# Optimization experiments

Hardware: AMD Instinct MI355X
Metric: run time of the kernel (lower is better)

Reference implementation:

```python
import jax, jax.numpy as jnp
import numpy as np

EMBED = 256
HEADS = 8
LEVELS = 4
POINTS = 4
HD = EMBED // HEADS  # 32
SHAPES = np.array([[100, 100], [50, 50], [25, 25], [13, 13]], dtype=np.int64)  # (H_l, W_l)


def setup_inputs() -> dict:
    key = jax.random.key(0)
    ks = jax.random.split(key, 12)
    nv = int(SHAPES.prod(-1).sum())  # 13294
    bs, nq, d = 2, nv, EMBED
    level_start = np.concatenate([[0], SHAPES.prod(-1).cumsum()[:-1]])
    s = 0.02
    return {
        "query": jax.random.normal(ks[0], (bs, nq, d), jnp.float32),
        "reference_points": jax.random.uniform(ks[1], (bs, nq, LEVELS, 2), jnp.float32),
        "value": jax.random.normal(ks[2], (bs, nv, d), jnp.float32),
        "spatial_shapes": jnp.asarray(SHAPES, jnp.int32),
        "level_start_index": jnp.asarray(level_start, jnp.int32),
        "key_padding_mask": jnp.zeros((bs, nv), jnp.bool_),
        "W_samp": jax.random.normal(ks[3], (HEADS * LEVELS * POINTS * 2, d), jnp.float32) * s,
        "b_samp": jax.random.normal(ks[4], (HEADS * LEVELS * POINTS * 2,), jnp.float32),
        "W_attn": jax.random.normal(ks[5], (HEADS * LEVELS * POINTS, d), jnp.float32) * s,
        "b_attn": jnp.zeros((HEADS * LEVELS * POINTS,), jnp.float32),
        "W_val": jax.random.normal(ks[6], (d, d), jnp.float32) * s,
        "b_val": jnp.zeros((d,), jnp.float32),
        "W_out": jax.random.normal(ks[7], (d, d), jnp.float32) * s,
        "b_out": jnp.zeros((d,), jnp.float32),
    }


def _msda_core(value_bhnd, shapes_np, starts_np, loc, attn):
    """value_bhnd: (bs, H, nv, hd); loc: (bs, nq, H, L, P, 2) in [0,1]; attn: (bs, nq, H, L, P)."""
    bs, heads, nv, hd = value_bhnd.shape
    nq = loc.shape[1]
    out = jnp.zeros((bs, nq, heads, hd), value_bhnd.dtype)
    for l in range(LEVELS):
        H, W = int(shapes_np[l, 0]), int(shapes_np[l, 1])
        start = int(starts_np[l])
        v = jax.lax.dynamic_slice_in_dim(value_bhnd, start, H * W, axis=2)  # (bs, heads, H*W, hd)
        # grid_sample(align_corners=False): pixel coord = loc * size - 0.5
        lx = loc[:, :, :, l, :, 0] * W - 0.5  # (bs, nq, heads, P)
        ly = loc[:, :, :, l, :, 1] * H - 0.5
        x0 = jnp.floor(lx)
        y0 = jnp.floor(ly)
        tx = lx - x0
        ty = ly - y0
        x0i = x0.astype(jnp.int32)
        y0i = y0.astype(jnp.int32)
        samp = jnp.zeros((bs, heads, nq, POINTS, hd), value_bhnd.dtype)
        for dy, wy in ((0, 1.0 - ty), (1, ty)):
            for dx, wx in ((0, 1.0 - tx), (1, tx)):
                xi = x0i + dx
                yi = y0i + dy
                valid = (xi >= 0) & (xi < W) & (yi >= 0) & (yi < H)  # zeros padding
                idx = jnp.clip(yi, 0, H - 1) * W + jnp.clip(xi, 0, W - 1)  # (bs, nq, heads, P)
                idx_t = idx.transpose(0, 2, 1, 3).reshape(bs, heads, nq * POINTS)
                g = jnp.take_along_axis(v, idx_t[..., None], axis=2)
                g = g.reshape(bs, heads, nq, POINTS, hd)
                w = jnp.where(valid, wx * wy, 0.0).transpose(0, 2, 1, 3)[..., None]
                samp = samp + g * w
        out = out + jnp.einsum("bhqpd,bqhp->bqhd", samp, attn[:, :, :, l, :])
    return out.reshape(bs, nq, heads * hd)


def reference(query, reference_points, value, spatial_shapes, level_start_index,
              key_padding_mask, W_samp, b_samp, W_attn, b_attn, W_val, b_val, W_out, b_out):
    bs, nq, d = query.shape
    v = value @ W_val.T + b_val
    v = jnp.where(key_padding_mask[..., None], 0.0, v)
    v = v.reshape(bs, -1, HEADS, HD).transpose(0, 2, 1, 3)  # (bs, heads, nv, hd)
    off = (query @ W_samp.T + b_samp).reshape(bs, nq, HEADS, LEVELS, POINTS, 2)
    attn = (query @ W_attn.T + b_attn).reshape(bs, nq, HEADS, LEVELS * POINTS)
    attn = jax.nn.softmax(attn, axis=-1).reshape(bs, nq, HEADS, LEVELS, POINTS)
    ss = np.asarray(spatial_shapes)
    starts = np.asarray(level_start_index)
    # offset normalizer is (W, H) per level
    norm = jnp.asarray(ss[:, ::-1].copy(), jnp.float32)
    loc = reference_points[:, :, None, :, None, :] + off / norm[None, None, None, :, None, :]
    out = _msda_core(v, ss, starts, loc, attn)
    return out @ W_out.T + b_out
```

## Files before the change

kernel.cpp:

```cpp
#include <hip/hip_runtime.h>
#include <hip/hip_bf16.h>
#include <hip/hip_fp16.h>
#include <cstdint>
#include <cstddef>

#define EMBED  256
#define NV_PER_B 13294
#define M_PAD   26624
#define NQPB   8

__constant__ const int c_H[4]  = {100, 50, 25, 13};
__constant__ const int c_W[4]  = {100, 50, 25, 13};
__constant__ const int c_ST[4] = {0, 10000, 12500, 13125};

typedef __attribute__((ext_vector_type(8))) short bf16x8;
typedef __attribute__((ext_vector_type(4))) float f32x4;

__device__ inline short f2bf(float x) {
    __hip_bfloat16 h = __float2bfloat16(x);
    return *reinterpret_cast<short*>(&h);
}

__global__ __launch_bounds__(256) void convert_kernel(
    const float* __restrict__ q,  const float* __restrict__ v,
    const float* __restrict__ wv, const float* __restrict__ wsamp,
    const float* __restrict__ wattn, const float* __restrict__ wo,
    const float* __restrict__ bsamp, const float* __restrict__ battn,
    short* __restrict__ q_bf, short* __restrict__ v_bf,
    short* __restrict__ wv_bf, short* __restrict__ wcat_bf,
    short* __restrict__ wo_bf, float* __restrict__ bias_cat,
    int n_real4, int n_pad4)
{
    const int i = blockIdx.x * 256 + threadIdx.x;
    if (i < n_pad4) {
        float4 a = make_float4(0.f, 0.f, 0.f, 0.f);
        float4 b = make_float4(0.f, 0.f, 0.f, 0.f);
        if (i < n_real4) {
            a = ((const float4*)q)[i];
            b = ((const float4*)v)[i];
        }
        ((short4*)q_bf)[i] = make_short4(f2bf(a.x), f2bf(a.y), f2bf(a.z), f2bf(a.w));
        ((short4*)v_bf)[i] = make_short4(f2bf(b.x), f2bf(b.y), f2bf(b.z), f2bf(b.w));
    }
    if (i < 16384) {
        float4 a = ((const float4*)wv)[i];
        float4 c = ((const float4*)wo)[i];
        ((short4*)wv_bf)[i] = make_short4(f2bf(a.x), f2bf(a.y), f2bf(a.z), f2bf(a.w));
        ((short4*)wo_bf)[i] = make_short4(f2bf(c.x), f2bf(c.y), f2bf(c.z), f2bf(c.w));
    }
    if (i < 24576) {
        float4 a = (i < 16384) ? ((const float4*)wsamp)[i]
                               : ((const float4*)wattn)[i - 16384];
        ((short4*)wcat_bf)[i] = make_short4(f2bf(a.x), f2bf(a.y), f2bf(a.z), f2bf(a.w));
    }
    if (i < 96) {
        float4 a = (i < 64) ? ((const float4*)bsamp)[i]
                            : ((const float4*)battn)[i - 64];
        ((float4*)bias_cat)[i] = a;
    }
}

__device__ __forceinline__ void gemm_kloop(
    const short* __restrict__ A, const short* __restrict__ Wt,
    int bm, int bn, char* smem, f32x4 (&acc)[4][4],
    int t, int wave, int lane)
{
    constexpr int K = 256;
    const int row0 = t >> 2, row1 = row0 + 64;
    const int kbl  = t & 3;
    const int kbg0 = kbl ^ (row0 & 3);
    const int kbg1 = kbl ^ (row1 & 3);
    const size_t a0 = (size_t)(bm + row0) * K + kbg0 * 8;
    const size_t a1 = (size_t)(bm + row1) * K + kbg1 * 8;
    const size_t b0 = (size_t)(bn + row0) * K + kbg0 * 8;
    const size_t b1 = (size_t)(bn + row1) * K + kbg1 * 8;
    const int lr16 = lane & 15, qk = lane >> 4;
    const int swz  = (qk ^ (lr16 & 3)) * 16;
    const int wrow = wave & 1, wcol = wave >> 1;

    auto issue = [&](int stage, int k0) {
        char* sa = smem + stage * 16384 + wave * 1024;
        char* sb = sa + 8192;
        __builtin_amdgcn_global_load_lds(
            (const __attribute__((address_space(1))) void*)(A + a0 + k0),
            (__attribute__((address_space(3))) void*)(sa), 16, 0, 0);
        __builtin_amdgcn_global_load_lds(
            (const __attribute__((address_space(1))) void*)(A + a1 + k0),
            (__attribute__((address_space(3))) void*)(sa + 4096), 16, 0, 0);
        __builtin_amdgcn_global_load_lds(
            (const __attribute__((address_space(1))) void*)(Wt + b0 + k0),
            (__attribute__((address_space(3))) void*)(sb), 16, 0, 0);
        __builtin_amdgcn_global_load_lds(
            (const __attribute__((address_space(1))) void*)(Wt + b1 + k0),
            (__attribute__((address_space(3))) void*)(sb + 4096), 16, 0, 0);
    };

    issue(0, 0);
    #pragma unroll
    for (int it = 0; it < 8; ++it) {
        __syncthreads();
        if (it + 1 < 8) issue((it + 1) & 1, (it + 1) * 32);
        const char* sa = smem + (it & 1) * 16384;
        const char* sb = sa + 8192;
        bf16x8 af[4], bfr[4];
        #pragma unroll
        for (int mi = 0; mi < 4; ++mi)
            af[mi] = *(const bf16x8*)(sa + (wrow * 64 + mi * 16 + lr16) * 64 + swz);
        #pragma unroll
        for (int ni = 0; ni < 4; ++ni)
            bfr[ni] = *(const bf16x8*)(sb + (wcol * 64 + ni * 16 + lr16) * 64 + swz);
        #pragma unroll
        for (int mi = 0; mi < 4; ++mi)
            #pragma unroll
            for (int ni = 0; ni < 4; ++ni)
                acc[mi][ni] = __builtin_amdgcn_mfma_f32_16x16x32_bf16(
                    af[mi], bfr[ni], acc[mi][ni], 0, 0, 0);
    }
}

__global__ __launch_bounds__(256) void gemm_mega_kernel(
    const short* __restrict__ v_bf, const short* __restrict__ wv_bf,
    const float* __restrict__ b_val, __half* __restrict__ vproj,
    const short* __restrict__ q_bf, const short* __restrict__ wcat_bf,
    const float* __restrict__ bias_cat, __half* __restrict__ qo)
{
    __shared__ __align__(16) char smem[36864];
    const int t = threadIdx.x;
    const int wave = t >> 6, lane = t & 63;
    const int lr16 = lane & 15, qk = lane >> 4;
    const int wrow = wave & 1, wcol = wave >> 1;
    const int y = blockIdx.y;
    const int bm = blockIdx.x * 128;

    const short* A; const short* Wt; const float* bias; __half* Cc; int Nst, bn;
    if (y < 2) { A = v_bf; Wt = wv_bf;   bias = b_val;    Cc = vproj; Nst = 256; bn = y * 128; }
    else       { A = q_bf; Wt = wcat_bf; bias = bias_cat; Cc = qo;    Nst = 384; bn = (y - 2) * 128; }

    f32x4 acc[4][4] = {};
    gemm_kloop(A, Wt, bm, bn, smem, acc, t, wave, lane);

    __syncthreads();
    __half* ep = (__half*)(smem + wave * 9216);
    const int colbase = bn + wcol * 64;
    float bv[4];
    #pragma unroll
    for (int ni = 0; ni < 4; ++ni) bv[ni] = bias[colbase + ni * 16 + lr16];
    #pragma unroll
    for (int mi = 0; mi < 4; ++mi)
        #pragma unroll
        for (int ni = 0; ni < 4; ++ni)
            #pragma unroll
            for (int r = 0; r < 4; ++r)
                ep[(mi * 16 + qk * 4 + r) * 72 + ni * 16 + lr16] =
                    __float2half(acc[mi][ni][r] + bv[ni]);
    __syncthreads();
    const int er = lane >> 3, ec = (lane & 7) * 8;
    #pragma unroll
    for (int pass = 0; pass < 8; ++pass) {
        const int r = pass * 8 + er;
        const int4 vv = *(const int4*)&ep[r * 72 + ec];
        const int grow = bm + wrow * 64 + r;
        *(int4*)&Cc[(size_t)grow * Nst + colbase + ec] = vv;
    }
}

__global__ __launch_bounds__(256) void gemm_out_kernel(
    const short* __restrict__ corebf, const short* __restrict__ wo_bf,
    const float* __restrict__ b_out, float* __restrict__ C, int M)
{
    __shared__ __align__(16) char smem[36864];
    const int t = threadIdx.x;
    const int wave = t >> 6, lane = t & 63;
    const int lr16 = lane & 15, qk = lane >> 4;
    const int wrow = wave & 1, wcol = wave >> 1;
    const int bm = blockIdx.x * 128, bn = blockIdx.y * 128;

    f32x4 acc[4][4] = {};
    gemm_kloop(corebf, wo_bf, bm, bn, smem, acc, t, wave, lane);

    const int colbase = bn + wcol * 64;
    float bv[4];
    #pragma unroll
    for (int ni = 0; ni < 4; ++ni) bv[ni] = b_out[colbase + ni * 16 + lr16];
    float* ep = (float*)(smem + wave * 8704);
    #pragma unroll
    for (int p = 0; p < 2; ++p) {
        __syncthreads();
        #pragma unroll
        for (int mh = 0; mh < 2; ++mh) {
            const int mi = p * 2 + mh;
            #pragma unroll
            for (int ni = 0; ni < 4; ++ni)
                #pragma unroll
                for (int r = 0; r < 4; ++r)
                    ep[(mh * 16 + qk * 4 + r) * 68 + ni * 16 + lr16] =
                        acc[mi][ni][r] + bv[ni];
        }
        __syncthreads();
        const int er = lane >> 4, ec = (lane & 15) * 4;
        #pragma unroll
        for (int j = 0; j < 8; ++j) {
            const int r = j * 4 + er;
            const float4 vv = *(const float4*)&ep[r * 68 + ec];
            const int grow = bm + wrow * 64 + p * 32 + r;
            if (grow < M)
                *(float4*)&C[(size_t)grow * 256 + colbase + ec] = vv;
        }
    }
}

__global__ __launch_bounds__(256) void msda_core_kernel(
    const __half* __restrict__ vproj,
    const float* __restrict__ refp,
    const __half* __restrict__ qo,
    short* __restrict__ core,
    int nq, int nv, int M)
{
    const int bq0 = blockIdx.x * NQPB;
    const int t = threadIdx.x;

    __shared__ float s_w[NQPB * 128];
    __shared__ float s_ref[NQPB * 8];
    __shared__ unsigned int s_tap[NQPB * 8][65];

    #pragma unroll
    for (int i = 0; i < 4; ++i) {
        const int s = t + i * 256;
        const int q = s >> 7, r = s & 127;
        s_w[s] = __half2float(qo[(size_t)(bq0 + q) * 384 + 256 + r]);
    }
    if (t < NQPB * 8) {
        const int gq = min(bq0 + (t >> 3), M - 1);
        s_ref[t] = refp[(size_t)gq * 8 + (t & 7)];
    }
    __syncthreads();

    if (t < NQPB * 8) {
        const int base = (t >> 3) * 128 + (t & 7) * 16;
        float m = -1e30f;
        #pragma unroll
        for (int j = 0; j < 16; ++j) m = fmaxf(m, s_w[base + j]);
        float e[16]; float ssum = 0.f;
        #pragma unroll
        for (int j = 0; j < 16; ++j) { e[j] = expf(s_w[base + j] - m); ssum += e[j]; }
        const float inv = 1.f / ssum;
        #pragma unroll
        for (int j = 0; j < 16; ++j) s_w[base + j] = e[j] * inv;
    }
    __syncthreads();

    #pragma unroll
    for (int i = 0; i < 4; ++i) {
        const int s = t + i * 256;
        const int q = s >> 7, r = s & 127;
        const int h = r >> 4, lp = r & 15, l = lp >> 2;
        const int gq = bq0 + q;
        const float2 off = __half22float2(*(const __half2*)&qo[(size_t)gq * 384 + r * 2]);
        const float rx = s_ref[q * 8 + l * 2];
        const float ry = s_ref[q * 8 + l * 2 + 1];
        const int W = c_W[l], H = c_H[l], st = c_ST[l];
        const float fW = (float)W, fH = (float)H;
        const float lx = (rx + off.x / fW) * fW - 0.5f;
        const float ly = (ry + off.y / fH) * fH - 0.5f;
        const float x0f = floorf(lx), y0f = floorf(ly);
        const float fx = lx - x0f, fy = ly - y0f;
        const int x0 = (int)x0f, y0 = (int)y0f;
        const float aw = s_w[s];
        const float wx[2] = {1.f - fx, fx};
        const float wy[2] = {1.f - fy, fy};
        #pragma unroll
        for (int dy = 0; dy < 2; ++dy) {
            #pragma unroll
            for (int dx = 0; dx < 2; ++dx) {
                const int xi = x0 + dx, yi = y0 + dy;
                const bool ok = (xi >= 0) & (xi < W) & (yi >= 0) & (yi < H);
                const unsigned int idx = ok ? (unsigned int)(st + yi * W + xi) : 0u;
                const float w = ok ? aw * wy[dy] * wx[dx] : 0.f;
                const unsigned int pw = (unsigned int)__half_as_ushort(__float2half(w));
                s_tap[q * 8 + h][lp * 4 + dy * 2 + dx] = idx | (pw << 16);
            }
        }
    }
    __syncthreads();

    const int q   = t >> 5;
    const int l32 = t & 31;
    const int h   = l32 >> 2;
    const int c8  = l32 & 3;
    const int gq  = bq0 + q;
    const int b   = (gq >= nq) ? 1 : 0;
    const __half* __restrict__ vb = vproj + (size_t)b * nv * EMBED + h * 32 + c8 * 8;
    const unsigned int* __restrict__ taps = s_tap[q * 8 + h];

    float a[8] = {0.f, 0.f, 0.f, 0.f, 0.f, 0.f, 0.f, 0.f};
    #pragma unroll 8
    for (int j = 0; j < 64; ++j) {
        const unsigned int u = taps[j];
        const float w = __half2float(__ushort_as_half((unsigned short)(u >> 16)));
        const int4 raw = *(const int4*)(vb + (size_t)(u & 0xFFFFu) * EMBED);
        const __half2* hh = (const __half2*)&raw;
        float2 f;
        f = __half22float2(hh[0]); a[0] = fmaf(w, f.x, a[0]); a[1] = fmaf(w, f.y, a[1]);
        f = __half22float2(hh[1]); a[2] = fmaf(w, f.x, a[2]); a[3] = fmaf(w, f.y, a[3]);
        f = __half22float2(hh[2]); a[4] = fmaf(w, f.x, a[4]); a[5] = fmaf(w, f.y, a[5]);
        f = __half22float2(hh[3]); a[6] = fmaf(w, f.x, a[6]); a[7] = fmaf(w, f.y, a[7]);
    }

    if (gq < M) {
        __align__(16) short o[8];
        #pragma unroll
        for (int i = 0; i < 8; ++i) o[i] = f2bf(a[i]);
        *(int4*)&core[(size_t)gq * 256 + h * 32 + c8 * 8] = *(const int4*)o;
    }
}

extern "C" void kernel_launch(void* const* d_in, const int* in_sizes, int n_in,
                              void* d_out, int out_size, void* d_ws, size_t ws_size,
                              hipStream_t stream) {
    const float* query  = (const float*)d_in[0];
    const float* refp   = (const float*)d_in[1];
    const float* value  = (const float*)d_in[2];
    const float* W_samp = (const float*)d_in[6];
    const float* b_samp = (const float*)d_in[7];
    const float* W_attn = (const float*)d_in[8];
    const float* b_attn = (const float*)d_in[9];
    const float* W_val  = (const float*)d_in[10];
    const float* b_val  = (const float*)d_in[11];
    const float* W_out  = (const float*)d_in[12];
    const float* b_out  = (const float*)d_in[13];
    float* out = (float*)d_out;

    const int M  = in_sizes[0] / EMBED;
    const int nq = NV_PER_B;
    const int nv = NV_PER_B;
    const int Mp = M_PAD;

    char* p = (char*)d_ws;
    short*  q_bf   = (short*)p;  p += (size_t)Mp * 256 * 2;
    short*  v_bf   = (short*)p;  p += (size_t)Mp * 256 * 2;
    short*  corebf = (short*)p;  p += (size_t)Mp * 256 * 2;
    __half* vproj  = (__half*)p; p += (size_t)Mp * 256 * 2;
    __half* qo     = (__half*)p; p += (size_t)Mp * 384 * 2;
    short*  wv_bf  = (short*)p;  p += 65536 * 2;
    short*  wcat   = (short*)p;  p += 98304 * 2;
    short*  wo_bf  = (short*)p;  p += 65536 * 2;
    float*  biascat= (float*)p;  p += 384 * 4;

    const int n_real4 = M * 256 / 4;
    const int n_pad4  = Mp * 256 / 4;
    dim3 blk(256);

    convert_kernel<<<dim3((n_pad4 + 255) / 256), blk, 0, stream>>>(
        query, value, W_val, W_samp, W_attn, W_out, b_samp, b_attn,
        q_bf, v_bf, wv_bf, wcat, wo_bf, biascat, n_real4, n_pad4);

    const int mb = Mp / 128;
    gemm_mega_kernel<<<dim3(mb, 5), blk, 0, stream>>>(
        v_bf, wv_bf, b_val, vproj, q_bf, wcat, biascat, qo);

    msda_core_kernel<<<dim3((M + NQPB - 1) / NQPB), blk, 0, stream>>>(
        vproj, refp, qo, corebf, nq, nv, M);

    gemm_out_kernel<<<dim3(mb, 2), blk, 0, stream>>>(
        corebf, wo_bf, b_out, out, M);
}
```

Before: 206.6 us.

## Switch GEMMs to fp16, per-wave LDS pipelines, and packed half2 sampling accumulation

Converts all intermediate buffers and MFMA from bf16 to fp16. The GEMM k-loop becomes per-wave: each wave stages its own tiles in private LDS with depth-2 prefetch and explicit waitcnts instead of block-wide __syncthreads. The MSDA gather loop reads four taps at once via uint4 and accumulates in half2 with hfma2, and the kernel gets an occupancy hint. Per-wave staging reloads shared tiles redundantly and doubles LDS use, and half-precision accumulation over 64 taps risks accuracy loss.

```diff
diff --git a/kernel.cpp b/kernel.cpp
--- a/kernel.cpp
+++ b/kernel.cpp
@@ -1,5 +1,4 @@
 #include <hip/hip_runtime.h>
-#include <hip/hip_bf16.h>
 #include <hip/hip_fp16.h>
 #include <cstdint>
 #include <cstddef>
@@ -13,22 +12,23 @@
 __constant__ const int c_W[4]  = {100, 50, 25, 13};
 __constant__ const int c_ST[4] = {0, 10000, 12500, 13125};
 
-typedef __attribute__((ext_vector_type(8))) short bf16x8;
-typedef __attribute__((ext_vector_type(4))) float f32x4;
-
-__device__ inline short f2bf(float x) {
-    __hip_bfloat16 h = __float2bfloat16(x);
-    return *reinterpret_cast<short*>(&h);
-}
+typedef _Float16 f16x8 __attribute__((ext_vector_type(8)));
+typedef float f32x4 __attribute__((ext_vector_type(4)));
+
+#define GLDS(g, l) __builtin_amdgcn_global_load_lds( \
+    (const __attribute__((address_space(1))) void*)(g), \
+    (__attribute__((address_space(3))) void*)(l), 16, 0, 0)
+
+__device__ inline unsigned short f2hu(float x) { return __half_as_ushort(__float2half(x)); }
 
 __global__ __launch_bounds__(256) void convert_kernel(
     const float* __restrict__ q,  const float* __restrict__ v,
     const float* __restrict__ wv, const float* __restrict__ wsamp,
     const float* __restrict__ wattn, const float* __restrict__ wo,
     const float* __restrict__ bsamp, const float* __restrict__ battn,
-    short* __restrict__ q_bf, short* __restrict__ v_bf,
-    short* __restrict__ wv_bf, short* __restrict__ wcat_bf,
-    short* __restrict__ wo_bf, float* __restrict__ bias_cat,
+    __half* __restrict__ q_h, __half* __restrict__ v_h,
+    __half* __restrict__ wv_h, __half* __restrict__ wcat_h,
+    __half* __restrict__ wo_h, float* __restrict__ bias_cat,
     int n_real4, int n_pad4)
 {
     const int i = blockIdx.x * 256 + threadIdx.x;
@@ -39,19 +39,19 @@
             a = ((const float4*)q)[i];
             b = ((const float4*)v)[i];
         }
-        ((short4*)q_bf)[i] = make_short4(f2bf(a.x), f2bf(a.y), f2bf(a.z), f2bf(a.w));
-        ((short4*)v_bf)[i] = make_short4(f2bf(b.x), f2bf(b.y), f2bf(b.z), f2bf(b.w));
+        ((ushort4*)q_h)[i] = make_ushort4(f2hu(a.x), f2hu(a.y), f2hu(a.z), f2hu(a.w));
+        ((ushort4*)v_h)[i] = make_ushort4(f2hu(b.x), f2hu(b.y), f2hu(b.z), f2hu(b.w));
     }
     if (i < 16384) {
         float4 a = ((const float4*)wv)[i];
         float4 c = ((const float4*)wo)[i];
-        ((short4*)wv_bf)[i] = make_short4(f2bf(a.x), f2bf(a.y), f2bf(a.z), f2bf(a.w));
-        ((short4*)wo_bf)[i] = make_short4(f2bf(c.x), f2bf(c.y), f2bf(c.z), f2bf(c.w));
+        ((ushort4*)wv_h)[i] = make_ushort4(f2hu(a.x), f2hu(a.y), f2hu(a.z), f2hu(a.w));
+        ((ushort4*)wo_h)[i] = make_ushort4(f2hu(c.x), f2hu(c.y), f2hu(c.z), f2hu(c.w));
     }
     if (i < 24576) {
         float4 a = (i < 16384) ? ((const float4*)wsamp)[i]
                                : ((const float4*)wattn)[i - 16384];
-        ((short4*)wcat_bf)[i] = make_short4(f2bf(a.x), f2bf(a.y), f2bf(a.z), f2bf(a.w));
+        ((ushort4*)wcat_h)[i] = make_ushort4(f2hu(a.x), f2hu(a.y), f2hu(a.z), f2hu(a.w));
     }
     if (i < 96) {
         float4 a = (i < 64) ? ((const float4*)bsamp)[i]
@@ -60,71 +60,53 @@
     }
 }
 
-__device__ __forceinline__ void gemm_kloop(
-    const short* __restrict__ A, const short* __restrict__ Wt,
-    int bm, int bn, char* smem, f32x4 (&acc)[4][4],
-    int t, int wave, int lane)
-{
-    constexpr int K = 256;
-    const int row0 = t >> 2, row1 = row0 + 64;
-    const int kbl  = t & 3;
-    const int kbg0 = kbl ^ (row0 & 3);
-    const int kbg1 = kbl ^ (row1 & 3);
-    const size_t a0 = (size_t)(bm + row0) * K + kbg0 * 8;
-    const size_t a1 = (size_t)(bm + row1) * K + kbg1 * 8;
-    const size_t b0 = (size_t)(bn + row0) * K + kbg0 * 8;
-    const size_t b1 = (size_t)(bn + row1) * K + kbg1 * 8;
-    const int lr16 = lane & 15, qk = lane >> 4;
-    const int swz  = (qk ^ (lr16 & 3)) * 16;
-    const int wrow = wave & 1, wcol = wave >> 1;
-
-    auto issue = [&](int stage, int k0) {
-        char* sa = smem + stage * 16384 + wave * 1024;
-        char* sb = sa + 8192;
-        __builtin_amdgcn_global_load_lds(
-            (const __attribute__((address_space(1))) void*)(A + a0 + k0),
-            (__attribute__((address_space(3))) void*)(sa), 16, 0, 0);
-        __builtin_amdgcn_global_load_lds(
-            (const __attribute__((address_space(1))) void*)(A + a1 + k0),
-            (__attribute__((address_space(3))) void*)(sa + 4096), 16, 0, 0);
-        __builtin_amdgcn_global_load_lds(
-            (const __attribute__((address_space(1))) void*)(Wt + b0 + k0),
-            (__attribute__((address_space(3))) void*)(sb), 16, 0, 0);
-        __builtin_amdgcn_global_load_lds(
-            (const __attribute__((address_space(1))) void*)(Wt + b1 + k0),
-            (__attribute__((address_space(3))) void*)(sb + 4096), 16, 0, 0);
+__device__ __forceinline__ void wave_kloop(
+    const __half* __restrict__ A, const __half* __restrict__ Wt,
+    size_t aoff, size_t boff, char* myst, f32x4 (&acc)[4][4],
+    int lr16, int qk)
+{
+    auto issue = [&](int stage, int kc) {
+        char* sa = myst + stage * 8192;
+        const __half* ap = A + aoff + kc * 32;
+        const __half* bp = Wt + boff + kc * 32;
+        #pragma unroll
+        for (int g = 0; g < 4; ++g) GLDS(ap + g * (16 * 256), sa + g * 1024);
+        #pragma unroll
+        for (int g = 0; g < 4; ++g) GLDS(bp + g * (16 * 256), sa + 4096 + g * 1024);
     };
 
     issue(0, 0);
+    issue(1, 1);
     #pragma unroll
     for (int it = 0; it < 8; ++it) {
-        __syncthreads();
-        if (it + 1 < 8) issue((it + 1) & 1, (it + 1) * 32);
-        const char* sa = smem + (it & 1) * 16384;
-        const char* sb = sa + 8192;
-        bf16x8 af[4], bfr[4];
+        if (it < 7) asm volatile("s_waitcnt vmcnt(8)" ::: "memory");
+        else        asm volatile("s_waitcnt vmcnt(0)" ::: "memory");
+        const char* sa = myst + (it & 1) * 8192;
+        f16x8 af[4], bfr[4];
         #pragma unroll
         for (int mi = 0; mi < 4; ++mi)
-            af[mi] = *(const bf16x8*)(sa + (wrow * 64 + mi * 16 + lr16) * 64 + swz);
+            af[mi] = *(const f16x8*)(sa + (mi * 16 + lr16) * 64 + qk * 16);
         #pragma unroll
         for (int ni = 0; ni < 4; ++ni)
-            bfr[ni] = *(const bf16x8*)(sb + (wcol * 64 + ni * 16 + lr16) * 64 + swz);
+            bfr[ni] = *(const f16x8*)(sa + 4096 + (ni * 16 + lr16) * 64 + qk * 16);
+        asm volatile("s_waitcnt lgkmcnt(0)" ::: "memory");
+        if (it + 2 < 8) issue(it & 1, it + 2);
         #pragma unroll
         for (int mi = 0; mi < 4; ++mi)
             #pragma unroll
             for (int ni = 0; ni < 4; ++ni)
-                acc[mi][ni] = __builtin_amdgcn_mfma_f32_16x16x32_bf16(
+                acc[mi][ni] = __builtin_amdgcn_mfma_f32_16x16x32_f16(
                     af[mi], bfr[ni], acc[mi][ni], 0, 0, 0);
     }
 }
 
-__global__ __launch_bounds__(256) void gemm_mega_kernel(
-    const short* __restrict__ v_bf, const short* __restrict__ wv_bf,
+__global__ __launch_bounds__(256) void proj_gemm_kernel(
+    const __half* __restrict__ v_h, const __half* __restrict__ wv_h,
     const float* __restrict__ b_val, __half* __restrict__ vproj,
-    const short* __restrict__ q_bf, const short* __restrict__ wcat_bf,
+    const __half* __restrict__ q_h, const __half* __restrict__ wcat_h,
     const float* __restrict__ bias_cat, __half* __restrict__ qo)
 {
-    __shared__ __align__(16) char smem[36864];
+    __shared__ __align__(16) char smem[65536];
     const int t = threadIdx.x;
     const int wave = t >> 6, lane = t & 63;
     const int lr16 = lane & 15, qk = lane >> 4;
@@ -132,19 +114,23 @@
     const int y = blockIdx.y;
     const int bm = blockIdx.x * 128;
 
-    const short* A; const short* Wt; const float* bias; __half* Cc; int Nst, bn;
-    if (y < 2) { A = v_bf; Wt = wv_bf;   bias = b_val;    Cc = vproj; Nst = 256; bn = y * 128; }
-    else       { A = q_bf; Wt = wcat_bf; bias = bias_cat; Cc = qo;    Nst = 384; bn = (y - 2) * 128; }
+    const __half* A; const __half* Wt; const float* bias; __half* Cc; int Nst, bn;
+    if (y < 2) { A = v_h; Wt = wv_h;   bias = b_val;    Cc = vproj; Nst = 256; bn = y * 128; }
+    else       { A = q_h; Wt = wcat_h; bias = bias_cat; Cc = qo;    Nst = 384; bn = (y - 2) * 128; }
+
+    char* myst = smem + wave * 16384;
+    const int srow = lane >> 2, skb = lane & 3;
+    const size_t aoff = (size_t)(bm + wrow * 64 + srow) * 256 + skb * 8;
+    const size_t boff = (size_t)(bn + wcol * 64 + srow) * 256 + skb * 8;
 
     f32x4 acc[4][4] = {};
-    gemm_kloop(A, Wt, bm, bn, smem, acc, t, wave, lane);
-
-    __syncthreads();
-    __half* ep = (__half*)(smem + wave * 9216);
+    wave_kloop(A, Wt, aoff, boff, myst, acc, lr16, qk);
+
     const int colbase = bn + wcol * 64;
     float bv[4];
     #pragma unroll
     for (int ni = 0; ni < 4; ++ni) bv[ni] = bias[colbase + ni * 16 + lr16];
+    __half* ep = (__half*)myst;
     #pragma unroll
     for (int mi = 0; mi < 4; ++mi)
         #pragma unroll
@@ -153,7 +139,6 @@
             for (int r = 0; r < 4; ++r)
                 ep[(mi * 16 + qk * 4 + r) * 72 + ni * 16 + lr16] =
                     __float2half(acc[mi][ni][r] + bv[ni]);
-    __syncthreads();
     const int er = lane >> 3, ec = (lane & 7) * 8;
     #pragma unroll
     for (int pass = 0; pass < 8; ++pass) {
@@ -165,55 +150,54 @@
 }
 
 __global__ __launch_bounds__(256) void gemm_out_kernel(
-    const short* __restrict__ corebf, const short* __restrict__ wo_bf,
+    const __half* __restrict__ core, const __half* __restrict__ wo_h,
     const float* __restrict__ b_out, float* __restrict__ C, int M)
 {
-    __shared__ __align__(16) char smem[36864];
+    __shared__ __align__(16) char smem[65536];
     const int t = threadIdx.x;
     const int wave = t >> 6, lane = t & 63;
     const int lr16 = lane & 15, qk = lane >> 4;
     const int wrow = wave & 1, wcol = wave >> 1;
     const int bm = blockIdx.x * 128, bn = blockIdx.y * 128;
 
+    char* myst = smem + wave * 16384;
+    const int srow = lane >> 2, skb = lane & 3;
+    const size_t aoff = (size_t)(bm + wrow * 64 + srow) * 256 + skb * 8;
+    const size_t boff = (size_t)(bn + wcol * 64 + srow) * 256 + skb * 8;
+
     f32x4 acc[4][4] = {};
-    gemm_kloop(corebf, wo_bf, bm, bn, smem, acc, t, wave, lane);
+    wave_kloop(core, wo_h, aoff, boff, myst, acc, lr16, qk);
 
     const int colbase = bn + wcol * 64;
     float bv[4];
     #pragma unroll
     for (int ni = 0; ni < 4; ++ni) bv[ni] = b_out[colbase + ni * 16 + lr16];
-    float* ep = (float*)(smem + wave * 8704);
-    #pragma unroll
-    for (int p = 0; p < 2; ++p) {
-        __syncthreads();
-        #pragma unroll
-        for (int mh = 0; mh < 2; ++mh) {
-            const int mi = p * 2 + mh;
+    float* ep = (float*)myst;
+    const int er = lane >> 4, ec = (lane & 15) * 4;
+    #pragma unroll
+    for (int p = 0; p < 4; ++p) {
+        #pragma unroll
+        for (int ni = 0; ni < 4; ++ni)
             #pragma unroll
-            for (int ni = 0; ni < 4; ++ni)
-                #pragma unroll
-                for (int r = 0; r < 4; ++r)
-                    ep[(mh * 16 + qk * 4 + r) * 68 + ni * 16 + lr16] =
-                        acc[mi][ni][r] + bv[ni];
-        }
-        __syncthreads();
-        const int er = lane >> 4, ec = (lane & 15) * 4;
-        #pragma unroll
-        for (int j = 0; j < 8; ++j) {
-            const int r = j * 4 + er;
-            const float4 vv = *(const float4*)&ep[r * 68 + ec];
-            const int grow = bm + wrow * 64 + p * 32 + r;
+            for (int r = 0; r < 4; ++r)
+                ep[(qk * 4 + r) * 68 + ni * 16 + lr16] = acc[p][ni][r] + bv[ni];
+        #pragma unroll
+        for (int j = 0; j < 4; ++j) {
+            const int r16 = j * 4 + er;
+            const float4 vv = *(const float4*)&ep[r16 * 68 + ec];
+            const int grow = bm + wrow * 64 + p * 16 + r16;
             if (grow < M)
                 *(float4*)&C[(size_t)grow * 256 + colbase + ec] = vv;
         }
-    }
-}
-
-__global__ __launch_bounds__(256) void msda_core_kernel(
+        asm volatile("s_waitcnt lgkmcnt(0)" ::: "memory");
+    }
+}
+
+__global__ __launch_bounds__(256, 4) void msda_core_kernel(
     const __half* __restrict__ vproj,
     const float* __restrict__ refp,
     const __half* __restrict__ qo,
-    short* __restrict__ core,
+    __half* __restrict__ core,
     int nq, int nv, int M)
 {
     const int bq0 = blockIdx.x * NQPB;
@@ -221,7 +205,7 @@
 
     __shared__ float s_w[NQPB * 128];
     __shared__ float s_ref[NQPB * 8];
-    __shared__ unsigned int s_tap[NQPB * 8][65];
+    __shared__ __align__(16) unsigned int s_tap[NQPB * 8][68];
 
     #pragma unroll
     for (int i = 0; i < 4; ++i) {
@@ -276,7 +260,7 @@
                 const bool ok = (xi >= 0) & (xi < W) & (yi >= 0) & (yi < H);
                 const unsigned int idx = ok ? (unsigned int)(st + yi * W + xi) : 0u;
                 const float w = ok ? aw * wy[dy] * wx[dx] : 0.f;
-                const unsigned int pw = (unsigned int)__half_as_ushort(__float2half(w));
+                const unsigned int pw = (unsigned int)f2hu(w);
                 s_tap[q * 8 + h][lp * 4 + dy * 2 + dx] = idx | (pw << 16);
             }
         }
@@ -290,28 +274,38 @@
     const int gq  = bq0 + q;
     const int b   = (gq >= nq) ? 1 : 0;
     const __half* __restrict__ vb = vproj + (size_t)b * nv * EMBED + h * 32 + c8 * 8;
-    const unsigned int* __restrict__ taps = s_tap[q * 8 + h];
-
-    float a[8] = {0.f, 0.f, 0.f, 0.f, 0.f, 0.f, 0.f, 0.f};
-    #pragma unroll 8
-    for (int j = 0; j < 64; ++j) {
-        const unsigned int u = taps[j];
-        const float w = __half2float(__ushort_as_half((unsigned short)(u >> 16)));
-        const int4 raw = *(const int4*)(vb + (size_t)(u & 0xFFFFu) * EMBED);
-        const __half2* hh = (const __half2*)&raw;
-        float2 f;
-        f = __half22float2(hh[0]); a[0] = fmaf(w, f.x, a[0]); a[1] = fmaf(w, f.y, a[1]);
-        f = __half22float2(hh[1]); a[2] = fmaf(w, f.x, a[2]); a[3] = fmaf(w, f.y, a[3]);
-        f = __half22float2(hh[2]); a[4] = fmaf(w, f.x, a[4]); a[5] = fmaf(w, f.y, a[5]);
-        f = __half22float2(hh[3]); a[6] = fmaf(w, f.x, a[6]); a[7] = fmaf(w, f.y, a[7]);
-    }
-
-    if (gq < M) {
-        __align__(16) short o[8];
-        #pragma unroll
-        for (int i = 0; i < 8; ++i) o[i] = f2bf(a[i]);
-        *(int4*)&core[(size_t)gq * 256 + h * 32 + c8 * 8] = *(const int4*)o;
-    }
+    const uint4* __restrict__ tapq = (const uint4*)s_tap[q * 8 + h];
+
+    __align__(16) __half2 acc2[4];
+    #pragma unroll
+    for (int i = 0; i < 4; ++i) acc2[i] = __float2half2_rn(0.f);
+
+    #pragma unroll 2
+    for (int g = 0; g < 16; ++g) {
+        const uint4 tq = tapq[g];
+        const int4 r0 = *(const int4*)(vb + (size_t)(tq.x & 0xFFFFu) * EMBED);
+        const int4 r1 = *(const int4*)(vb + (size_t)(tq.y & 0xFFFFu) * EMBED);
+        const int4 r2 = *(const int4*)(vb + (size_t)(tq.z & 0xFFFFu) * EMBED);
+        const int4 r3 = *(const int4*)(vb + (size_t)(tq.w & 0xFFFFu) * EMBED);
+        const __half2 w0 = __half2half2(__ushort_as_half((unsigned short)(tq.x >> 16)));
+        const __half2 w1 = __half2half2(__ushort_as_half((unsigned short)(tq.y >> 16)));
+        const __half2 w2 = __half2half2(__ushort_as_half((unsigned short)(tq.z >> 16)));
+        const __half2 w3 = __half2half2(__ushort_as_half((unsigned short)(tq.w >> 16)));
+        const __half2* h0 = (const __half2*)&r0;
+        const __half2* h1 = (const __half2*)&r1;
+        const __half2* h2 = (const __half2*)&r2;
+        const __half2* h3 = (const __half2*)&r3;
+        #pragma unroll
+        for (int i = 0; i < 4; ++i) {
+            acc2[i] = __hfma2(w0, h0[i], acc2[i]);
+            acc2[i] = __hfma2(w1, h1[i], acc2[i]);
+            acc2[i] = __hfma2(w2, h2[i], acc2[i]);
+            acc2[i] = __hfma2(w3, h3[i], acc2[i]);
+        }
+    }
+
+    if (gq < M)
+        *(int4*)&core[(size_t)gq * 256 + h * 32 + c8 * 8] = *(const int4*)acc2;
 }
 
 extern "C" void kernel_launch(void* const* d_in, const int* in_sizes, int n_in,
@@ -336,14 +330,14 @@
     const int Mp = M_PAD;
 
     char* p = (char*)d_ws;
-    short*  q_bf   = (short*)p;  p += (size_t)Mp * 256 * 2;
-    short*  v_bf   = (short*)p;  p += (size_t)Mp * 256 * 2;
-    short*  corebf = (short*)p;  p += (size_t)Mp * 256 * 2;
+    __half* coreh  = (__half*)p; p += (size_t)Mp * 256 * 2;
     __half* vproj  = (__half*)p; p += (size_t)Mp * 256 * 2;
     __half* qo     = (__half*)p; p += (size_t)Mp * 384 * 2;
-    short*  wv_bf  = (short*)p;  p += 65536 * 2;
-    short*  wcat   = (short*)p;  p += 98304 * 2;
-    short*  wo_bf  = (short*)p;  p += 65536 * 2;
+    __half* q_h    = (__half*)p; p += (size_t)Mp * 256 * 2;
+    __half* v_h    = (__half*)p; p += (size_t)Mp * 256 * 2;
+    __half* wv_h   = (__half*)p; p += 65536 * 2;
+    __half* wcat_h = (__half*)p; p += 98304 * 2;
+    __half* wo_h   = (__half*)p; p += 65536 * 2;
     float*  biascat= (float*)p;  p += 384 * 4;
 
     const int n_real4 = M * 256 / 4;
@@ -352,15 +346,15 @@
 
     convert_kernel<<<dim3((n_pad4 + 255) / 256), blk, 0, stream>>>(
         query, value, W_val, W_samp, W_attn, W_out, b_samp, b_attn,
-        q_bf, v_bf, wv_bf, wcat, wo_bf, biascat, n_real4, n_pad4);
+        q_h, v_h, wv_h, wcat_h, wo_h, biascat, n_real4, n_pad4);
 
     const int mb = Mp / 128;
-    gemm_mega_kernel<<<dim3(mb, 5), blk, 0, stream>>>(
-        v_bf, wv_bf, b_val, vproj, q_bf, wcat, biascat, qo);
+    proj_gemm_kernel<<<dim3(mb, 5), blk, 0, stream>>>(
+        v_h, wv_h, b_val, vproj, q_h, wcat_h, biascat, qo);
 
     msda_core_kernel<<<dim3((M + NQPB - 1) / NQPB), blk, 0, stream>>>(
-        vproj, refp, qo, corebf, nq, nv, M);
+        vproj, refp, qo, coreh, nq, nv, M);
 
     gemm_out_kernel<<<dim3(mb, 2), blk, 0, stream>>>(
-        corebf, wo_bf, b_out, out, M);
-}
+        coreh, wo_h, b_out, out, M);
+}
```

Measured after the change: 206.7 us. About the same (+0.1%).
